# Performance work log

Hardware: AMD Instinct MI355X
Metric: run time of the kernel (lower is better)

## Reference

```python
import jax, jax.numpy as jnp
import numpy as np

LAM = 10.0          # lam_val from __init__ (cp.Constant)
N_ITERS = 100       # fixed FISTA iterations; converges to QP solution (kappa ~ 1+16*LAM)


def _dtd(v):
    """Apply D^T D where D is the (n-2, n) second-difference operator, along last axis."""
    d = v[..., 2:] - 2.0 * v[..., 1:-1] + v[..., :-2]            # D v, shape (..., n-2)
    pad = [(0, 0)] * (v.ndim - 1) + [(2, 2)]
    dp = jnp.pad(d, pad)                                          # zero-pad for adjoint
    return dp[..., 2:] - 2.0 * dp[..., 1:-1] + dp[..., :-2]      # D^T d, shape (..., n)


def _solve_rows(y):
    """Batched QP:  min ||y - x||^2 + LAM * ||diff(x, 2)||^2  s.t.  0 <= x <= y,
    solved independently along the last axis via projected accelerated gradient (FISTA).
    Hessian/2 = I + LAM * D^T D, lambda_max(D^T D) <= 16 -> Lipschitz L = 2*(1 + 16*LAM).
    """
    step = 1.0 / (2.0 * (1.0 + 16.0 * LAM))
    proj = lambda v: jnp.clip(v, 0.0, y)   # box projection onto [0, y]
    x0 = proj(y)

    def body(i, carry):
        x, z, t = carry
        g = 2.0 * (z - y) + (2.0 * LAM) * _dtd(z)
        x_new = proj(z - step * g)
        t_new = 0.5 * (1.0 + jnp.sqrt(1.0 + 4.0 * t * t))
        z_new = x_new + ((t - 1.0) / t_new) * (x_new - x)
        return (x_new, z_new, t_new)

    x, _, _ = jax.lax.fori_loop(0, N_ITERS, body, (x0, x0, jnp.float32(1.0)))
    return x


def setup_inputs() -> dict:
    key = jax.random.key(0)
    # Batch of images in [0,1] (like normalized MNIST); constraint 0 <= x <= y is feasible.
    data = jax.random.uniform(key, (32, 512, 512), dtype=jnp.float32)
    return {"data": data}


def reference(data):
    # Pass 1: denoise each row of each image.
    pass1 = _solve_rows(data)
    # Pass 2: the original call() transposes a numpy VIEW and writes in place, so its
    # "column" pass actually re-solves the SAME rows (with y = pass-1 output) and the
    # final transpose undoes itself. We replicate that exact math.
    pass2 = _solve_rows(pass1)
    b, h, w = pass2.shape
    return pass2.reshape(b, h, w, 1)
```

## Files before the change

kernel.cpp:

```cpp
#include <hip/hip_runtime.h>
#include <math.h>

#define ROW_N 512
#define N_ITERS 100
#define LAMBDA 10.0f

typedef float f2 __attribute__((ext_vector_type(2)));

__device__ __forceinline__ f2 splat(float s) { f2 r; r.x = s; r.y = s; return r; }
__device__ __forceinline__ f2 ffma(f2 a, f2 b, f2 c) {
    return __builtin_elementwise_fma(a, b, c);
}

__global__ void coef_kernel(float* __restrict__ coefs) {
    if (threadIdx.x == 0) {
        float t = 1.0f;
        for (int k = 0; k < N_ITERS; ++k) {
            float t_new = 0.5f * (1.0f + sqrtf(1.0f + 4.0f * t * t));
            coefs[k] = (t - 1.0f) / t_new;
            t = t_new;
        }
    }
}

template <bool USE_TABLE>
__global__ __launch_bounds__(256)
__attribute__((amdgpu_waves_per_eu(2, 8)))
void fista_kernel(
    const float* __restrict__ in, float* __restrict__ out,
    const float* __restrict__ coefs, int n_rows)
{
    const int pid  = (int)((blockIdx.x * 256u + threadIdx.x) >> 6);
    const int lane = (int)(threadIdx.x & 63u);
    const int n_pairs = (n_rows + 1) >> 1;
    if (pid >= n_pairs) return;

    const bool lane_lo = (lane == 0);
    const bool lane_hi = (lane == 63);

    const int r0 = pid * 2;
    const int r1 = (r0 + 1 < n_rows) ? r0 + 1 : r0;
    const float* rowA = in + (size_t)r0 * ROW_N + lane * 8;
    const float* rowB = in + (size_t)r1 * ROW_N + lane * 8;

    const float A = 1.0f / (1.0f + 16.0f * LAMBDA);
    const float B = LAMBDA / (1.0f + 16.0f * LAMBDA);
    const float C = 1.0f - A;
    const f2 K0 = splat(C - 6.0f * B);
    const f2 B4 = splat(4.0f * B);
    const f2 Bn = splat(-B);
    const f2 Av = splat(A);
    const f2 TWO = splat(2.0f);

    f2 y[8], ay[8], xA[8], xB[8], z[8];
    {
        const float4 a0 = *(const float4*)(rowA);
        const float4 a1 = *(const float4*)(rowA + 4);
        const float4 b0 = *(const float4*)(rowB);
        const float4 b1 = *(const float4*)(rowB + 4);
        y[0].x = a0.x; y[1].x = a0.y; y[2].x = a0.z; y[3].x = a0.w;
        y[4].x = a1.x; y[5].x = a1.y; y[6].x = a1.z; y[7].x = a1.w;
        y[0].y = b0.x; y[1].y = b0.y; y[2].y = b0.z; y[3].y = b0.w;
        y[4].y = b1.x; y[5].y = b1.y; y[6].y = b1.z; y[7].y = b1.w;
    }

    f2 zm1, zm2, sp0, sp1;

    auto upd = [&](int i, f2 a, f2 b, f2 c, f2 d,
                   const f2* xin, f2* xout, float cf) {
        f2 t1 = a + b;
        f2 t2 = c + d;
        f2 u = ffma(K0, z[i], ay[i]);
        u = ffma(B4, t1, u);
        u = ffma(Bn, t2, u);
        f2 xe;
        xe.x = __builtin_amdgcn_fmed3f(u.x, 0.0f, y[i].x);
        xe.y = __builtin_amdgcn_fmed3f(u.y, 0.0f, y[i].y);
        f2 dd = xe - xin[i];
        f2 zn;
        zn.x = fmaf(cf, dd.x, xe.x);
        zn.y = fmaf(cf, dd.y, xe.y);
        z[i] = zn;
        xout[i] = xe;
    };

    auto step = [&](const f2* xin, f2* xout, float cf) {
        const f2 z2o = z[2], z3o = z[3], z4o = z[4], z5o = z[5];
        upd(2, z[1], z[3], z[0], z[4], xin, xout, cf);
        upd(3, z2o,  z[4], z[1], z[5], xin, xout, cf);
        upd(4, z3o,  z[5], z2o,  z[6], xin, xout, cf);
        upd(5, z4o,  z[6], z3o,  z[7], xin, xout, cf);

        f2 gp0 = ffma(TWO, z[7], -z[6]);
        f2 gp1 = ffma(TWO, gp0, -z[7]);
        f2 zp0, zp1;
        zp0.x = lane_hi ? gp0.x : sp0.x;  zp0.y = lane_hi ? gp0.y : sp0.y;
        zp1.x = lane_hi ? gp1.x : sp1.x;  zp1.y = lane_hi ? gp1.y : sp1.y;

        const f2 z6o = z[6];
        upd(6, z5o, z[7], z4o, zp0, xin, xout, cf);
        upd(7, z6o, zp0,  z5o, zp1, xin, xout, cf);

        f2 um1, um2;
        um2.x = __shfl_up(z[6].x, 1); um2.y = __shfl_up(z[6].y, 1);
        um1.x = __shfl_up(z[7].x, 1); um1.y = __shfl_up(z[7].y, 1);

        const f2 z0o = z[0];
        upd(0, zm1, z[1], zm2, z2o, xin, xout, cf);
        upd(1, z0o, z2o,  zm1, z3o, xin, xout, cf);

        f2 gm1 = ffma(TWO, z[0], -z[1]);
        f2 gm2 = ffma(TWO, gm1, -z[0]);
        zm1.x = lane_lo ? gm1.x : um1.x;  zm1.y = lane_lo ? gm1.y : um1.y;
        zm2.x = lane_lo ? gm2.x : um2.x;  zm2.y = lane_lo ? gm2.y : um2.y;

        sp0.x = __shfl_down(z[0].x, 1); sp0.y = __shfl_down(z[0].y, 1);
        sp1.x = __shfl_down(z[1].x, 1); sp1.y = __shfl_down(z[1].y, 1);
    };

    #pragma unroll 1
    for (int pass = 0; pass < 2; ++pass) {
        #pragma unroll
        for (int i = 0; i < 8; ++i) {
            ay[i] = Av * y[i];
            xA[i] = y[i];
            z[i]  = y[i];
        }
        {
            f2 um1, um2;
            um2.x = __shfl_up(z[6].x, 1); um2.y = __shfl_up(z[6].y, 1);
            um1.x = __shfl_up(z[7].x, 1); um1.y = __shfl_up(z[7].y, 1);
            f2 gm1 = ffma(TWO, z[0], -z[1]);
            f2 gm2 = ffma(TWO, gm1, -z[0]);
            zm1.x = lane_lo ? gm1.x : um1.x;  zm1.y = lane_lo ? gm1.y : um1.y;
            zm2.x = lane_lo ? gm2.x : um2.x;  zm2.y = lane_lo ? gm2.y : um2.y;
            sp0.x = __shfl_down(z[0].x, 1); sp0.y = __shfl_down(z[0].y, 1);
            sp1.x = __shfl_down(z[1].x, 1); sp1.y = __shfl_down(z[1].y, 1);
        }

        float tcur = 1.0f;
        #pragma unroll 1
        for (int it = 0; it < N_ITERS; it += 2) {
            float c0, c1;
            if (USE_TABLE) {
                c0 = coefs[it];
                c1 = coefs[it + 1];
            } else {
                float tn  = 0.5f * (1.0f + sqrtf(fmaf(4.0f * tcur, tcur, 1.0f)));
                c0 = (tcur - 1.0f) / tn;
                float tn2 = 0.5f * (1.0f + sqrtf(fmaf(4.0f * tn, tn, 1.0f)));
                c1 = (tn - 1.0f) / tn2;
                tcur = tn2;
            }
            step(xA, xB, c0);
            step(xB, xA, c1);
        }

        if (pass == 0) {
            #pragma unroll
            for (int i = 0; i < 8; ++i) y[i] = xA[i];
        }
    }

    float* orowA = out + (size_t)r0 * ROW_N + lane * 8;
    *(float4*)(orowA)     = make_float4(xA[0].x, xA[1].x, xA[2].x, xA[3].x);
    *(float4*)(orowA + 4) = make_float4(xA[4].x, xA[5].x, xA[6].x, xA[7].x);
    if (r1 > r0) {
        float* orowB = out + (size_t)r1 * ROW_N + lane * 8;
        *(float4*)(orowB)     = make_float4(xA[0].y, xA[1].y, xA[2].y, xA[3].y);
        *(float4*)(orowB + 4) = make_float4(xA[4].y, xA[5].y, xA[6].y, xA[7].y);
    }
}

extern "C" void kernel_launch(void* const* d_in, const int* in_sizes, int n_in,
                              void* d_out, int out_size, void* d_ws, size_t ws_size,
                              hipStream_t stream) {
    const float* in = (const float*)d_in[0];
    float* out = (float*)d_out;

    const int total   = in_sizes[0];
    const int n_rows  = total / ROW_N;
    const int n_pairs = (n_rows + 1) >> 1;
    const int waves_per_block = 4;
    const int blocks = (n_pairs + waves_per_block - 1) / waves_per_block;

    if (ws_size >= N_ITERS * sizeof(float)) {
        float* coefs = (float*)d_ws;
        coef_kernel<<<1, 64, 0, stream>>>(coefs);
        fista_kernel<true><<<blocks, 256, 0, stream>>>(in, out, coefs, n_rows);
    } else {
        fista_kernel<false><<<blocks, 256, 0, stream>>>(in, out, nullptr, n_rows);
    }
}
```

Measured before the change: 345.0 us.

## Map one row per wavefront, use ds_bpermute shuffles, prefetch coefficients

Drops the two-rows-per-wave packed f2 scheme and assigns one row per wavefront, doubling the wave count and raising the waves_per_eu hint to 4. Lane shuffles become explicit ds_bpermute calls with precomputed addresses, and the FISTA coefficients for the next iteration pair are loaded one iteration ahead. The aim is more waves to hide shuffle and memory latency, at the cost of losing packed-FMA throughput and issuing twice as many cross-lane ops per row.

```diff
diff --git a/kernel.cpp b/kernel.cpp
--- a/kernel.cpp
+++ b/kernel.cpp
@@ -4,13 +4,6 @@
 #define ROW_N 512
 #define N_ITERS 100
 #define LAMBDA 10.0f
-
-typedef float f2 __attribute__((ext_vector_type(2)));
-
-__device__ __forceinline__ f2 splat(float s) { f2 r; r.x = s; r.y = s; return r; }
-__device__ __forceinline__ f2 ffma(f2 a, f2 b, f2 c) {
-    return __builtin_elementwise_fma(a, b, c);
-}
 
 __global__ void coef_kernel(float* __restrict__ coefs) {
     if (threadIdx.x == 0) {
@@ -23,137 +16,135 @@
     }
 }
 
+__device__ __forceinline__ float lane_gather(int byte_addr, float v) {
+    return __int_as_float(__builtin_amdgcn_ds_bpermute(byte_addr, __float_as_int(v)));
+}
+
 template <bool USE_TABLE>
 __global__ __launch_bounds__(256)
-__attribute__((amdgpu_waves_per_eu(2, 8)))
+__attribute__((amdgpu_waves_per_eu(4, 8)))
 void fista_kernel(
     const float* __restrict__ in, float* __restrict__ out,
     const float* __restrict__ coefs, int n_rows)
 {
-    const int pid  = (int)((blockIdx.x * 256u + threadIdx.x) >> 6);
+    const int wid  = (int)((blockIdx.x * 256u + threadIdx.x) >> 6);
     const int lane = (int)(threadIdx.x & 63u);
-    const int n_pairs = (n_rows + 1) >> 1;
-    if (pid >= n_pairs) return;
+    if (wid >= n_rows) return;
 
     const bool lane_lo = (lane == 0);
     const bool lane_hi = (lane == 63);
+    const int addr_up = ((lane - 1) & 63) << 2;
+    const int addr_dn = ((lane + 1) & 63) << 2;
 
-    const int r0 = pid * 2;
-    const int r1 = (r0 + 1 < n_rows) ? r0 + 1 : r0;
-    const float* rowA = in + (size_t)r0 * ROW_N + lane * 8;
-    const float* rowB = in + (size_t)r1 * ROW_N + lane * 8;
+    const float* row = in + (size_t)wid * ROW_N + lane * 8;
 
-    const float A = 1.0f / (1.0f + 16.0f * LAMBDA);
-    const float B = LAMBDA / (1.0f + 16.0f * LAMBDA);
-    const float C = 1.0f - A;
-    const f2 K0 = splat(C - 6.0f * B);
-    const f2 B4 = splat(4.0f * B);
-    const f2 Bn = splat(-B);
-    const f2 Av = splat(A);
-    const f2 TWO = splat(2.0f);
+    const float A  = 1.0f / (1.0f + 16.0f * LAMBDA);
+    const float B  = LAMBDA / (1.0f + 16.0f * LAMBDA);
+    const float C  = 1.0f - A;
+    const float K0 = C - 6.0f * B;
+    const float B4 = 4.0f * B;
+    const float Bn = -B;
 
-    f2 y[8], ay[8], xA[8], xB[8], z[8];
+    float y[8], ay[8], xA[8], xB[8], z[8];
     {
-        const float4 a0 = *(const float4*)(rowA);
-        const float4 a1 = *(const float4*)(rowA + 4);
-        const float4 b0 = *(const float4*)(rowB);
-        const float4 b1 = *(const float4*)(rowB + 4);
-        y[0].x = a0.x; y[1].x = a0.y; y[2].x = a0.z; y[3].x = a0.w;
-        y[4].x = a1.x; y[5].x = a1.y; y[6].x = a1.z; y[7].x = a1.w;
-        y[0].y = b0.x; y[1].y = b0.y; y[2].y = b0.z; y[3].y = b0.w;
-        y[4].y = b1.x; y[5].y = b1.y; y[6].y = b1.z; y[7].y = b1.w;
+        const float4 a0 = *(const float4*)(row);
+        const float4 a1 = *(const float4*)(row + 4);
+        y[0] = a0.x; y[1] = a0.y; y[2] = a0.z; y[3] = a0.w;
+        y[4] = a1.x; y[5] = a1.y; y[6] = a1.z; y[7] = a1.w;
     }
 
-    f2 zm1, zm2, sp0, sp1;
+    float zm1, zm2, sp0, sp1;
 
-    auto upd = [&](int i, f2 a, f2 b, f2 c, f2 d,
-                   const f2* xin, f2* xout, float cf) {
-        f2 t1 = a + b;
-        f2 t2 = c + d;
-        f2 u = ffma(K0, z[i], ay[i]);
-        u = ffma(B4, t1, u);
-        u = ffma(Bn, t2, u);
-        f2 xe;
-        xe.x = __builtin_amdgcn_fmed3f(u.x, 0.0f, y[i].x);
-        xe.y = __builtin_amdgcn_fmed3f(u.y, 0.0f, y[i].y);
-        f2 dd = xe - xin[i];
-        f2 zn;
-        zn.x = fmaf(cf, dd.x, xe.x);
-        zn.y = fmaf(cf, dd.y, xe.y);
-        z[i] = zn;
+    auto upd = [&](int i, float a, float b, float c, float d,
+                   const float* xin, float* xout, float cf) {
+        float t1 = a + b;
+        float t2 = c + d;
+        float u  = fmaf(K0, z[i], ay[i]);
+        u = fmaf(B4, t1, u);
+        u = fmaf(Bn, t2, u);
+        float xe = __builtin_amdgcn_fmed3f(u, 0.0f, y[i]);
+        z[i] = fmaf(cf, xe - xin[i], xe);
         xout[i] = xe;
     };
 
-    auto step = [&](const f2* xin, f2* xout, float cf) {
-        const f2 z2o = z[2], z3o = z[3], z4o = z[4], z5o = z[5];
+    auto step = [&](const float* xin, float* xout, float cf) {
+        const float z2o = z[2], z3o = z[3], z4o = z[4], z5o = z[5];
         upd(2, z[1], z[3], z[0], z[4], xin, xout, cf);
         upd(3, z2o,  z[4], z[1], z[5], xin, xout, cf);
         upd(4, z3o,  z[5], z2o,  z[6], xin, xout, cf);
         upd(5, z4o,  z[6], z3o,  z[7], xin, xout, cf);
 
-        f2 gp0 = ffma(TWO, z[7], -z[6]);
-        f2 gp1 = ffma(TWO, gp0, -z[7]);
-        f2 zp0, zp1;
-        zp0.x = lane_hi ? gp0.x : sp0.x;  zp0.y = lane_hi ? gp0.y : sp0.y;
-        zp1.x = lane_hi ? gp1.x : sp1.x;  zp1.y = lane_hi ? gp1.y : sp1.y;
+        float gp0 = fmaf(2.0f, z[7], -z[6]);
+        float gp1 = fmaf(2.0f, gp0, -z[7]);
+        float zp0 = lane_hi ? gp0 : sp0;
+        float zp1 = lane_hi ? gp1 : sp1;
 
-        const f2 z6o = z[6];
+        const float z6o = z[6];
         upd(6, z5o, z[7], z4o, zp0, xin, xout, cf);
         upd(7, z6o, zp0,  z5o, zp1, xin, xout, cf);
 
-        f2 um1, um2;
-        um2.x = __shfl_up(z[6].x, 1); um2.y = __shfl_up(z[6].y, 1);
-        um1.x = __shfl_up(z[7].x, 1); um1.y = __shfl_up(z[7].y, 1);
+        float um2 = lane_gather(addr_up, z[6]);
+        float um1 = lane_gather(addr_up, z[7]);
 
-        const f2 z0o = z[0];
+        const float z0o = z[0];
         upd(0, zm1, z[1], zm2, z2o, xin, xout, cf);
         upd(1, z0o, z2o,  zm1, z3o, xin, xout, cf);
 
-        f2 gm1 = ffma(TWO, z[0], -z[1]);
-        f2 gm2 = ffma(TWO, gm1, -z[0]);
-        zm1.x = lane_lo ? gm1.x : um1.x;  zm1.y = lane_lo ? gm1.y : um1.y;
-        zm2.x = lane_lo ? gm2.x : um2.x;  zm2.y = lane_lo ? gm2.y : um2.y;
+        float gm1 = fmaf(2.0f, z[0], -z[1]);
+        float gm2 = fmaf(2.0f, gm1, -z[0]);
+        zm1 = lane_lo ? gm1 : um1;
+        zm2 = lane_lo ? gm2 : um2;
 
-        sp0.x = __shfl_down(z[0].x, 1); sp0.y = __shfl_down(z[0].y, 1);
-        sp1.x = __shfl_down(z[1].x, 1); sp1.y = __shfl_down(z[1].y, 1);
+        sp0 = lane_gather(addr_dn, z[0]);
+        sp1 = lane_gather(addr_dn, z[1]);
     };
 
     #pragma unroll 1
     for (int pass = 0; pass < 2; ++pass) {
         #pragma unroll
         for (int i = 0; i < 8; ++i) {
-            ay[i] = Av * y[i];
+            ay[i] = A * y[i];
             xA[i] = y[i];
             z[i]  = y[i];
         }
         {
-            f2 um1, um2;
-            um2.x = __shfl_up(z[6].x, 1); um2.y = __shfl_up(z[6].y, 1);
-            um1.x = __shfl_up(z[7].x, 1); um1.y = __shfl_up(z[7].y, 1);
-            f2 gm1 = ffma(TWO, z[0], -z[1]);
-            f2 gm2 = ffma(TWO, gm1, -z[0]);
-            zm1.x = lane_lo ? gm1.x : um1.x;  zm1.y = lane_lo ? gm1.y : um1.y;
-            zm2.x = lane_lo ? gm2.x : um2.x;  zm2.y = lane_lo ? gm2.y : um2.y;
-            sp0.x = __shfl_down(z[0].x, 1); sp0.y = __shfl_down(z[0].y, 1);
-            sp1.x = __shfl_down(z[1].x, 1); sp1.y = __shfl_down(z[1].y, 1);
+            float um2 = lane_gather(addr_up, z[6]);
+            float um1 = lane_gather(addr_up, z[7]);
+            float gm1 = fmaf(2.0f, z[0], -z[1]);
+            float gm2 = fmaf(2.0f, gm1, -z[0]);
+            zm1 = lane_lo ? gm1 : um1;
+            zm2 = lane_lo ? gm2 : um2;
+            sp0 = lane_gather(addr_dn, z[0]);
+            sp1 = lane_gather(addr_dn, z[1]);
         }
 
-        float tcur = 1.0f;
+        float c0, c1, tcur = 1.0f;
+        if (USE_TABLE) { c0 = coefs[0]; c1 = coefs[1]; }
+        else {
+            float tn = 0.5f * (1.0f + sqrtf(fmaf(4.0f * tcur, tcur, 1.0f)));
+            c0 = (tcur - 1.0f) / tn;
+            float tn2 = 0.5f * (1.0f + sqrtf(fmaf(4.0f * tn, tn, 1.0f)));
+            c1 = (tn - 1.0f) / tn2;
+            tcur = tn2;
+        }
+
         #pragma unroll 1
         for (int it = 0; it < N_ITERS; it += 2) {
-            float c0, c1;
+            float n0, n1;
             if (USE_TABLE) {
-                c0 = coefs[it];
-                c1 = coefs[it + 1];
+                const int j = (it + 2 < N_ITERS) ? it + 2 : 0;
+                n0 = coefs[j];
+                n1 = coefs[j + 1];
             } else {
-                float tn  = 0.5f * (1.0f + sqrtf(fmaf(4.0f * tcur, tcur, 1.0f)));
-                c0 = (tcur - 1.0f) / tn;
+                float tn = 0.5f * (1.0f + sqrtf(fmaf(4.0f * tcur, tcur, 1.0f)));
+                n0 = (tcur - 1.0f) / tn;
                 float tn2 = 0.5f * (1.0f + sqrtf(fmaf(4.0f * tn, tn, 1.0f)));
-                c1 = (tn - 1.0f) / tn2;
+                n1 = (tn - 1.0f) / tn2;
                 tcur = tn2;
             }
             step(xA, xB, c0);
             step(xB, xA, c1);
+            c0 = n0; c1 = n1;
         }
 
         if (pass == 0) {
@@ -162,14 +153,9 @@
         }
     }
 
-    float* orowA = out + (size_t)r0 * ROW_N + lane * 8;
-    *(float4*)(orowA)     = make_float4(xA[0].x, xA[1].x, xA[2].x, xA[3].x);
-    *(float4*)(orowA + 4) = make_float4(xA[4].x, xA[5].x, xA[6].x, xA[7].x);
-    if (r1 > r0) {
-        float* orowB = out + (size_t)r1 * ROW_N + lane * 8;
-        *(float4*)(orowB)     = make_float4(xA[0].y, xA[1].y, xA[2].y, xA[3].y);
-        *(float4*)(orowB + 4) = make_float4(xA[4].y, xA[5].y, xA[6].y, xA[7].y);
-    }
+    float* orow = out + (size_t)wid * ROW_N + lane * 8;
+    *(float4*)(orow)     = make_float4(xA[0], xA[1], xA[2], xA[3]);
+    *(float4*)(orow + 4) = make_float4(xA[4], xA[5], xA[6], xA[7]);
 }
 
 extern "C" void kernel_launch(void* const* d_in, const int* in_sizes, int n_in,
@@ -178,11 +164,10 @@
     const float* in = (const float*)d_in[0];
     float* out = (float*)d_out;
 
-    const int total   = in_sizes[0];
-    const int n_rows  = total / ROW_N;
-    const int n_pairs = (n_rows + 1) >> 1;
+    const int total  = in_sizes[0];
+    const int n_rows = total / ROW_N;
     const int waves_per_block = 4;
-    const int blocks = (n_pairs + waves_per_block - 1) / waves_per_block;
+    const int blocks = (n_rows + waves_per_block - 1) / waves_per_block;
 
     if (ws_size >= N_ITERS * sizeof(float)) {
         float* coefs = (float*)d_ws;
```

Result: slower. 394.7 us (+14.4%).

## Use DPP wave shifts for halo exchange and prefetch FISTA coefficients

Applied to the files above, without the earlier changes.

Replaces the ds_bpermute-based __shfl_up/__shfl_down halo exchange and lane-0/lane-63 selects with DPP wave_shr/wave_shl moves. The boundary reflection values serve as the DPP 'old' operand, so edge lanes pick them up with no extra select. The per-step update order becomes a simple sequential sweep with all halos built after the step, and the z update uses packed f2 FMA. Coefficient loads are software-pipelined one iteration ahead, hiding global-load latency in the serial loop. The risk is that the sequential order adds a dependency stall on DPP results, and that wave-wide DPP shift controls must match the hardware's support.

```diff
diff --git a/kernel.cpp b/kernel.cpp
--- a/kernel.cpp
+++ b/kernel.cpp
@@ -10,6 +10,19 @@
 __device__ __forceinline__ f2 splat(float s) { f2 r; r.x = s; r.y = s; return r; }
 __device__ __forceinline__ f2 ffma(f2 a, f2 b, f2 c) {
     return __builtin_elementwise_fma(a, b, c);
+}
+
+#define DPP_WAVE_SHL1 0x130
+#define DPP_WAVE_SHR1 0x138
+
+template <int CTRL>
+__device__ __forceinline__ f2 dpp2(f2 old, f2 src) {
+    f2 r;
+    r.x = __int_as_float(__builtin_amdgcn_update_dpp(
+        __float_as_int(old.x), __float_as_int(src.x), CTRL, 0xF, 0xF, false));
+    r.y = __int_as_float(__builtin_amdgcn_update_dpp(
+        __float_as_int(old.y), __float_as_int(src.y), CTRL, 0xF, 0xF, false));
+    return r;
 }
 
 __global__ void coef_kernel(float* __restrict__ coefs) {
@@ -34,9 +47,6 @@
     const int lane = (int)(threadIdx.x & 63u);
     const int n_pairs = (n_rows + 1) >> 1;
     if (pid >= n_pairs) return;
-
-    const bool lane_lo = (lane == 0);
-    const bool lane_hi = (lane == 63);
 
     const int r0 = pid * 2;
     const int r1 = (r0 + 1 < n_rows) ? r0 + 1 : r0;
@@ -64,10 +74,21 @@
         y[4].y = b1.x; y[5].y = b1.y; y[6].y = b1.z; y[7].y = b1.w;
     }
 
-    f2 zm1, zm2, sp0, sp1;
+    f2 zm1, zm2, zp0, zp1;
+
+    auto make_halos = [&]() {
+        f2 gm1 = ffma(TWO, z[0], -z[1]);
+        f2 gm2 = ffma(TWO, gm1, -z[0]);
+        f2 gp0 = ffma(TWO, z[7], -z[6]);
+        f2 gp1 = ffma(TWO, gp0, -z[7]);
+        zm1 = dpp2<DPP_WAVE_SHR1>(gm1, z[7]);
+        zm2 = dpp2<DPP_WAVE_SHR1>(gm2, z[6]);
+        zp0 = dpp2<DPP_WAVE_SHL1>(gp0, z[0]);
+        zp1 = dpp2<DPP_WAVE_SHL1>(gp1, z[1]);
+    };
 
     auto upd = [&](int i, f2 a, f2 b, f2 c, f2 d,
-                   const f2* xin, f2* xout, float cf) {
+                   const f2* xin, f2* xout, f2 cf) {
         f2 t1 = a + b;
         f2 t2 = c + d;
         f2 u = ffma(K0, z[i], ay[i]);
@@ -76,46 +97,23 @@
         f2 xe;
         xe.x = __builtin_amdgcn_fmed3f(u.x, 0.0f, y[i].x);
         xe.y = __builtin_amdgcn_fmed3f(u.y, 0.0f, y[i].y);
-        f2 dd = xe - xin[i];
-        f2 zn;
-        zn.x = fmaf(cf, dd.x, xe.x);
-        zn.y = fmaf(cf, dd.y, xe.y);
-        z[i] = zn;
+        z[i] = ffma(cf, xe - xin[i], xe);
         xout[i] = xe;
     };
 
-    auto step = [&](const f2* xin, f2* xout, float cf) {
-        const f2 z2o = z[2], z3o = z[3], z4o = z[4], z5o = z[5];
-        upd(2, z[1], z[3], z[0], z[4], xin, xout, cf);
-        upd(3, z2o,  z[4], z[1], z[5], xin, xout, cf);
-        upd(4, z3o,  z[5], z2o,  z[6], xin, xout, cf);
-        upd(5, z4o,  z[6], z3o,  z[7], xin, xout, cf);
-
-        f2 gp0 = ffma(TWO, z[7], -z[6]);
-        f2 gp1 = ffma(TWO, gp0, -z[7]);
-        f2 zp0, zp1;
-        zp0.x = lane_hi ? gp0.x : sp0.x;  zp0.y = lane_hi ? gp0.y : sp0.y;
-        zp1.x = lane_hi ? gp1.x : sp1.x;  zp1.y = lane_hi ? gp1.y : sp1.y;
-
-        const f2 z6o = z[6];
-        upd(6, z5o, z[7], z4o, zp0, xin, xout, cf);
-        upd(7, z6o, zp0,  z5o, zp1, xin, xout, cf);
-
-        f2 um1, um2;
-        um2.x = __shfl_up(z[6].x, 1); um2.y = __shfl_up(z[6].y, 1);
-        um1.x = __shfl_up(z[7].x, 1); um1.y = __shfl_up(z[7].y, 1);
-
-        const f2 z0o = z[0];
-        upd(0, zm1, z[1], zm2, z2o, xin, xout, cf);
-        upd(1, z0o, z2o,  zm1, z3o, xin, xout, cf);
-
-        f2 gm1 = ffma(TWO, z[0], -z[1]);
-        f2 gm2 = ffma(TWO, gm1, -z[0]);
-        zm1.x = lane_lo ? gm1.x : um1.x;  zm1.y = lane_lo ? gm1.y : um1.y;
-        zm2.x = lane_lo ? gm2.x : um2.x;  zm2.y = lane_lo ? gm2.y : um2.y;
-
-        sp0.x = __shfl_down(z[0].x, 1); sp0.y = __shfl_down(z[0].y, 1);
-        sp1.x = __shfl_down(z[1].x, 1); sp1.y = __shfl_down(z[1].y, 1);
+    auto step = [&](const f2* xin, f2* xout, float cfs) {
+        const f2 cf = splat(cfs);
+        f2 o0 = z[0], o1 = z[1], o2 = z[2], o3 = z[3], o4 = z[4],
+           o5 = z[5], o6 = z[6];
+        upd(0, zm1, z[1], zm2, z[2], xin, xout, cf);
+        upd(1, o0,  z[2], zm1, z[3], xin, xout, cf);
+        upd(2, o1,  z[3], o0,  z[4], xin, xout, cf);
+        upd(3, o2,  z[4], o1,  z[5], xin, xout, cf);
+        upd(4, o3,  z[5], o2,  z[6], xin, xout, cf);
+        upd(5, o4,  z[6], o3,  z[7], xin, xout, cf);
+        upd(6, o5,  z[7], o4,  zp0,  xin, xout, cf);
+        upd(7, o6,  zp0,  o5,  zp1,  xin, xout, cf);
+        make_halos();
     };
 
     #pragma unroll 1
@@ -126,34 +124,35 @@
             xA[i] = y[i];
             z[i]  = y[i];
         }
-        {
-            f2 um1, um2;
-            um2.x = __shfl_up(z[6].x, 1); um2.y = __shfl_up(z[6].y, 1);
-            um1.x = __shfl_up(z[7].x, 1); um1.y = __shfl_up(z[7].y, 1);
-            f2 gm1 = ffma(TWO, z[0], -z[1]);
-            f2 gm2 = ffma(TWO, gm1, -z[0]);
-            zm1.x = lane_lo ? gm1.x : um1.x;  zm1.y = lane_lo ? gm1.y : um1.y;
-            zm2.x = lane_lo ? gm2.x : um2.x;  zm2.y = lane_lo ? gm2.y : um2.y;
-            sp0.x = __shfl_down(z[0].x, 1); sp0.y = __shfl_down(z[0].y, 1);
-            sp1.x = __shfl_down(z[1].x, 1); sp1.y = __shfl_down(z[1].y, 1);
+        make_halos();
+
+        float c0, c1, tcur = 1.0f;
+        if (USE_TABLE) { c0 = coefs[0]; c1 = coefs[1]; }
+        else {
+            float tn = 0.5f * (1.0f + sqrtf(fmaf(4.0f * tcur, tcur, 1.0f)));
+            c0 = (tcur - 1.0f) / tn;
+            float tn2 = 0.5f * (1.0f + sqrtf(fmaf(4.0f * tn, tn, 1.0f)));
+            c1 = (tn - 1.0f) / tn2;
+            tcur = tn2;
         }
 
-        float tcur = 1.0f;
         #pragma unroll 1
         for (int it = 0; it < N_ITERS; it += 2) {
-            float c0, c1;
+            float n0, n1;
             if (USE_TABLE) {
-                c0 = coefs[it];
-                c1 = coefs[it + 1];
+                const int j = (it + 2 < N_ITERS) ? it + 2 : 0;
+                n0 = coefs[j];
+                n1 = coefs[j + 1];
             } else {
-                float tn  = 0.5f * (1.0f + sqrtf(fmaf(4.0f * tcur, tcur, 1.0f)));
-                c0 = (tcur - 1.0f) / tn;
+                float tn = 0.5f * (1.0f + sqrtf(fmaf(4.0f * tcur, tcur, 1.0f)));
+                n0 = (tcur - 1.0f) / tn;
                 float tn2 = 0.5f * (1.0f + sqrtf(fmaf(4.0f * tn, tn, 1.0f)));
-                c1 = (tn - 1.0f) / tn2;
+                n1 = (tn - 1.0f) / tn2;
                 tcur = tn2;
             }
             step(xA, xB, c0);
             step(xB, xA, c1);
+            c0 = n0; c1 = n1;
         }
 
         if (pass == 0) {
```

New measurement: 344.8 us. No clear change (-0.1%).
